# Kernel tuning notes

Hardware: AMD Instinct MI355X
Metric: run time of the kernel (lower is better)

## Reference

```python
import jax, jax.numpy as jnp
import numpy as np

# ---- fixed config (matches A_Sp_P4CNN cfg with n_channels=32) ----
C = 32          # n_channels
B = 32          # batch
H = W = 48      # input spatial size
KS = 3          # main conv kernel
SPK = 7         # spatial-attention kernel
EPS = 2e-5      # BatchNorm eps
NG = 4          # p4 rotation group size (n_grid)
SAME7 = [(SPK // 2, SPK // 2)] * 2  # 'same' padding for attention convs


def _conv2d(x, w, padding):
    return jax.lax.conv_general_dilated(
        x, w, window_strides=(1, 1), padding=padding,
        dimension_numbers=('NCHW', 'OIHW', 'NCHW'))


def _rot(w, r):
    # rotate kernel spatially by r*90 deg (p4 group action on Z2 kernels)
    return jnp.rot90(w, k=r, axes=(-2, -1))


def _gg_rot(w, r):
    # p4 action on a GG kernel [O,I,4,k,k]: spatial rotation + cyclic shift of
    # the input-rotation axis
    return jnp.roll(_rot(w, r), shift=r, axis=2)


def _lift_conv(x, w, padding):
    # lifting conv Z2 -> p4: x [B,Ci,H,W], w [Co,Ci,k,k] -> [B,Co,4,H',W']
    return jnp.stack([_conv2d(x, _rot(w, r), padding) for r in range(NG)], axis=2)


def _gg_conv(x, w, padding):
    # group conv p4 -> p4: x [B,Ci,4,H,W], w [Co,Ci,4,k,k] -> [B,Co,4,H',W']
    b, ci, g, h, ww = x.shape
    xf = x.reshape(b, ci * g, h, ww)
    outs = []
    for r in range(NG):
        wr = _gg_rot(w, r).reshape(w.shape[0], ci * g, w.shape[-2], w.shape[-1])
        outs.append(_conv2d(xf, wr, padding))
    return jnp.stack(outs, axis=2)


def _sp_att_rng(x, aw):
    # CBAM-style spatial attention lifted to p4: [B,Ci,H,W] -> [B,1,4,H,W]
    a = jnp.concatenate([jnp.mean(x, 1, keepdims=True),
                         jnp.max(x, 1, keepdims=True)], axis=1)
    return jax.nn.sigmoid(_lift_conv(a, aw, SAME7))


def _sp_att_gg(x, aw):
    # spatial attention on a p4 feature map: [B,Ci,4,H,W] -> [B,1,4,H,W]
    a = jnp.concatenate([jnp.mean(x, 1, keepdims=True),
                         jnp.max(x, 1, keepdims=True)], axis=1)
    return jax.nn.sigmoid(_gg_conv(a, aw, SAME7))


def _att_conv_rng(x, w, bias, aw):
    # attentive lifting conv: per output rotation r, modulate the input with the
    # r-th spatial attention map, then convolve with the r-rotated kernel
    att = _sp_att_rng(x, aw)  # [B,1,4,H,W]
    outs = [_conv2d(att[:, :, r] * x, _rot(w, r), 'VALID') for r in range(NG)]
    return jnp.stack(outs, axis=2) + bias[None, :, None, None, None]


def _att_conv_gg(x, w, bias, aw):
    # attentive group conv: attention broadcast over channels + input rotations
    att = _sp_att_gg(x, aw)  # [B,1,4,H,W]
    b, ci, g, h, ww = x.shape
    outs = []
    for r in range(NG):
        xr = (att[:, :, r][:, :, None] * x).reshape(b, ci * g, h, ww)
        wr = _gg_rot(w, r).reshape(w.shape[0], ci * g, KS, KS)
        outs.append(_conv2d(xr, wr, 'VALID'))
    return jnp.stack(outs, axis=2) + bias[None, :, None, None, None]


def _bn3d(x, gamma, beta):
    # BatchNorm3d over [B,C,4,H,W]: per-channel stats over (B,4,H,W) (training-mode math)
    m = jnp.mean(x, axis=(0, 2, 3, 4), keepdims=True)
    v = jnp.var(x, axis=(0, 2, 3, 4), keepdims=True)
    return gamma[None, :, None, None, None] * (x - m) * jax.lax.rsqrt(v + EPS) \
        + beta[None, :, None, None, None]


def _max_pool2(x):
    # max_pooling_Rn: 2x2/2 spatial max pool on [B,C,4,H,W]
    return jax.lax.reduce_window(x, -jnp.inf, jax.lax.max,
                                 (1, 1, 1, 2, 2), (1, 1, 1, 2, 2), 'VALID')


def setup_inputs() -> dict:
    key = jax.random.key(0)
    ks = jax.random.split(key, 40)
    sd = 0.1
    inp = {'x': jax.random.normal(ks[0], (B, 1, H, W), dtype=jnp.float32)}
    # c1: lifting conv 1 -> C
    inp['w1'] = jax.random.normal(ks[1], (C, 1, KS, KS), dtype=jnp.float32) * sd
    inp['b1'] = jnp.zeros((C,), jnp.float32)
    inp['aw1'] = jax.random.normal(ks[2], (1, 2, SPK, SPK), dtype=jnp.float32) * sd
    # c2..c6: GG convs C -> C
    for i in range(2, 7):
        inp[f'w{i}'] = jax.random.normal(ks[3 * i], (C, C, NG, KS, KS), dtype=jnp.float32) * sd
        inp[f'b{i}'] = jnp.zeros((C,), jnp.float32)
        inp[f'aw{i}'] = jax.random.normal(ks[3 * i + 1], (1, 2, NG, SPK, SPK), dtype=jnp.float32) * sd
    # c7: GG conv C -> 10 (classifier)
    inp['w7'] = jax.random.normal(ks[30], (10, C, NG, KS, KS), dtype=jnp.float32) * sd
    inp['b7'] = jnp.zeros((10,), jnp.float32)
    inp['aw7'] = jax.random.normal(ks[31], (1, 2, NG, SPK, SPK), dtype=jnp.float32) * sd
    # BatchNorm3d affine params bn1..bn6
    for i in range(1, 7):
        inp[f'g{i}'] = jnp.ones((C,), jnp.float32)
        inp[f'be{i}'] = jnp.zeros((C,), jnp.float32)
    return inp


def reference(x, w1, b1, aw1, w2, b2, aw2, w3, b3, aw3, w4, b4, aw4,
              w5, b5, aw5, w6, b6, aw6, w7, b7, aw7,
              g1, be1, g2, be2, g3, be3, g4, be4, g5, be5, g6, be6):
    # dropout is identity in eval-mode reference
    out = jax.nn.relu(_bn3d(_att_conv_rng(x, w1, b1, aw1), g1, be1))
    out = jax.nn.relu(_bn3d(_att_conv_gg(out, w2, b2, aw2), g2, be2))
    out = _max_pool2(out)
    out = jax.nn.relu(_bn3d(_att_conv_gg(out, w3, b3, aw3), g3, be3))
    out = jax.nn.relu(_bn3d(_att_conv_gg(out, w4, b4, aw4), g4, be4))
    out = jax.nn.relu(_bn3d(_att_conv_gg(out, w5, b5, aw5), g5, be5))
    out = jax.nn.relu(_bn3d(_att_conv_gg(out, w6, b6, aw6), g6, be6))
    out = _att_conv_gg(out, w7, b7, aw7)  # [B,10,4,h,w]
    out = jnp.max(out, axis=2)            # pool over rotation group (dim=-3)
    out = jnp.mean(out, axis=(2, 3))      # adaptive_avg_pool2d(1) + view
    return out                             # [B,10]
```

## Files before the change

kernel.cpp:

```cpp
#include <hip/hip_runtime.h>
#include <cstddef>

#define DINL static __device__ __forceinline__

typedef __attribute__((ext_vector_type(4))) float f4v;
typedef __attribute__((ext_vector_type(8))) short bh8;
typedef __attribute__((ext_vector_type(4))) unsigned short us4;

DINL void rot_src(int r, int K, int i, int j, int& si, int& sj) {
  switch (r & 3) {
    case 0:  si = i;       sj = j;       break;
    case 1:  si = j;       sj = K-1-i;   break;
    case 2:  si = K-1-i;   sj = K-1-j;   break;
    default: si = K-1-j;   sj = i;       break;
  }
}

DINL float sigmoidf(float s) { return 1.f / (1.f + __expf(-s)); }

DINL unsigned short f2bf(float f) {
  unsigned u = __builtin_bit_cast(unsigned, f);
  u += 0x7fffu + ((u >> 16) & 1u);
  return (unsigned short)(u >> 16);
}
DINL float bf2f(unsigned short h) {
  unsigned u = ((unsigned)h) << 16;
  return __builtin_bit_cast(float, u);
}

__global__ void k_prep_w(const float* __restrict__ w2, const float* __restrict__ w3,
                         const float* __restrict__ w4, const float* __restrict__ w5,
                         const float* __restrict__ w6, const float* __restrict__ w7,
                         unsigned short* __restrict__ wrot) {
  int idx = blockIdx.x * 256 + threadIdx.x;
  if (idx >= 811008) return;
  const float* w; int OM, O, base;
  if (idx < 737280) {
    int L = idx / 147456; base = L * 147456; OM = 2; O = 32;
    w = (L == 0) ? w2 : (L == 1) ? w3 : (L == 2) ? w4 : (L == 3) ? w5 : w6;
  } else { base = 737280; OM = 1; O = 10; w = w7; }
  int local = idx - base;
  int j = local & 7; int t = local >> 3;
  int lanei = t & 63; t >>= 6;
  int mi = t % OM; t /= OM;
  int ks = t & 3; t >>= 2;
  int tap = t % 9; int r = t / 9;
  int n = lanei & 15, q = lanei >> 4;
  int o = mi * 16 + n;
  int ci = q * 8 + j;
  int gs = (ks - r) & 3;
  int ky = tap / 3, kx = tap % 3;
  int si, sj; rot_src(r, 3, ky, kx, si, sj);
  float val = (o < O) ? w[((o * 32 + ci) * 4 + gs) * 9 + si * 3 + sj] : 0.f;
  wrot[idx] = f2bf(val);
}

DINL void bn_finalize_par(const float* __restrict__ partl,
                          const float* __restrict__ gamma, const float* __restrict__ beta,
                          float* st, float* l1, float* l2, int npix, int tid) {
  if (tid < 256) {
    int c = tid & 31, grp = tid >> 5;
    float s1 = 0.f, s2 = 0.f;
    #pragma unroll
    for (int k = 0; k < 8; ++k) {
      int bk = grp * 8 + k;
      s1 += partl[bk * 128 + c];
      s2 += partl[bk * 128 + 64 + c];
    }
    l1[tid] = s1; l2[tid] = s2;
  }
  __syncthreads();
  if (tid < 32) {
    float a = 0.f, q = 0.f;
    #pragma unroll
    for (int k = 0; k < 8; ++k) { a += l1[k * 32 + tid]; q += l2[k * 32 + tid]; }
    float N = 4.f * (float)npix;
    float m = a / N;
    float v = q / N - m * m;
    float inv = rsqrtf(v + 2e-5f);
    float sc = gamma[tid] * inv;
    st[tid] = sc;
    st[32 + tid] = beta[tid] - m * sc;
  }
  __syncthreads();
}

__global__ void __launch_bounds__(256)
k_att_lift(const float* __restrict__ x, const float* __restrict__ aw,
           float* __restrict__ att) {
  const int H = 48, HW = H * H;
  __shared__ float wsum[4][49];
  for (int i = threadIdx.x; i < 196; i += 256) {
    int r = i / 49; int t = i % 49;
    int ky = t / 7, kx = t % 7;
    int si, sj; rot_src(r, 7, ky, kx, si, sj);
    wsum[r][t] = aw[si * 7 + sj] + aw[49 + si * 7 + sj];
  }
  __syncthreads();
  int idx = blockIdx.x * 256 + threadIdx.x;
  if (idx >= 32 * 4 * HW) return;
  int xw = idx % H; int t = idx / H;
  int yh = t % H;  t /= H;
  int r  = t & 3;  int b = t >> 2;
  const float* xb = x + b * HW;
  float s = 0.f;
  for (int ky = 0; ky < 7; ++ky) {
    int y = yh + ky - 3;
    if ((unsigned)y >= (unsigned)H) continue;
    for (int kx = 0; kx < 7; ++kx) {
      int xx = xw + kx - 3;
      if ((unsigned)xx >= (unsigned)H) continue;
      s += xb[y * H + xx] * wsum[r][ky * 7 + kx];
    }
  }
  att[idx] = sigmoidf(s);
}

__global__ void __launch_bounds__(256)
k_conv_lift(const float* __restrict__ x, const float* __restrict__ att,
            const float* __restrict__ w, const float* __restrict__ bias,
            unsigned short* __restrict__ y, float* __restrict__ partl) {
  const int HO = 46;
  __shared__ float xs[3 * 48];
  __shared__ float as[4][3 * 48];
  __shared__ float wsm[288];
  __shared__ float bs[32];
  __shared__ float bnred[64];
  int id = blockIdx.x;
  int yo = id % HO; int b = id / HO;

  for (int i = threadIdx.x; i < 144; i += 256)
    xs[i] = x[b * 2304 + (yo + i / 48) * 48 + (i % 48)];
  for (int i = threadIdx.x; i < 576; i += 256) {
    int r = i / 144; int rem = i % 144;
    as[r][rem] = att[(b * 4 + r) * 2304 + (yo + rem / 48) * 48 + (rem % 48)];
  }
  for (int i = threadIdx.x; i < 288; i += 256) wsm[i] = w[i];
  if (threadIdx.x < 32) bs[threadIdx.x] = bias[threadIdx.x];
  if (threadIdx.x < 64) bnred[threadIdx.x] = 0.f;
  __syncthreads();

  int o = threadIdx.x & 31;
  int cl = threadIdx.x >> 5;
  float wreg[9];
  #pragma unroll
  for (int i = 0; i < 9; ++i) wreg[i] = wsm[o * 9 + i];
  float bv = bs[o];
  float sacc = 0.f, qacc = 0.f;

  for (int c8 = 0; c8 < 6; ++c8) {
    int col = c8 * 8 + cl;
    if (col < HO) {
      float xv[9];
      #pragma unroll
      for (int ky = 0; ky < 3; ++ky)
        #pragma unroll
        for (int kx = 0; kx < 3; ++kx)
          xv[ky * 3 + kx] = xs[ky * 48 + col + kx];
      unsigned short* yp = y + ((size_t)b * 2116 + yo * HO + col) * 128 + o;
      #pragma unroll
      for (int r = 0; r < 4; ++r) {
        float acc = bv;
        #pragma unroll
        for (int ky = 0; ky < 3; ++ky)
          #pragma unroll
          for (int kx = 0; kx < 3; ++kx) {
            int si, sj; rot_src(r, 3, ky, kx, si, sj);
            acc = fmaf(as[r][ky * 48 + col + kx] * xv[ky * 3 + kx], wreg[si * 3 + sj], acc);
          }
        yp[r * 32] = f2bf(acc);
        sacc += acc; qacc += acc * acc;
      }
    }
  }
  atomicAdd(&bnred[o], sacc);
  atomicAdd(&bnred[32 + o], qacc);
  __syncthreads();
  if (threadIdx.x < 64) {
    int bucket = blockIdx.x & 63;
    int c = threadIdx.x & 31;
    int off = (threadIdx.x < 32) ? c : (64 + c);
    atomicAdd(&partl[bucket * 128 + off], bnred[threadIdx.x]);
  }
}

template<int H, int OM, int O, int OSTR, bool BNS>
__global__ void __launch_bounds__(256)
k_conv_mfma(const unsigned short* __restrict__ xn, const float* __restrict__ att,
            const unsigned short* __restrict__ wl, const float* __restrict__ bias,
            unsigned short* __restrict__ y, float* __restrict__ partl) {
  constexpr int HO = H - 2, HW = H * H;
  constexpr int TR = 8, TC = 16, WR = TR + 2, WC = TC + 2, CGH = 68;
  constexpr int NRT = (HO + TR - 1) / TR, NCT = (HO + TC - 1) / TC;
  __shared__ __align__(16) unsigned short xa[WR * WC * CGH];
  __shared__ float bnred[128];

  int id = blockIdx.x;
  int slot = id & 7; int k = id >> 3;
  int tile = k % (NRT * NCT); k /= (NRT * NCT);
  int r = k & 3; int bhi = k >> 2;
  int b = bhi * 8 + slot;
  int rt = tile / NCT, ct = tile % NCT;
  int row0 = rt * TR, c0 = ct * TC;

  const unsigned short* xb = xn + (size_t)b * HW * 128;
  const float* ab = att + (size_t)(b * 4 + r) * HW;

  int lane = threadIdx.x & 63;
  int wv = threadIdx.x >> 6;
  int n = lane & 15, quad = lane >> 4;

  f4v acc[OM][2];
  #pragma unroll
  for (int mi = 0; mi < OM; ++mi)
    #pragma unroll
    for (int ri = 0; ri < 2; ++ri) {
      acc[mi][ri][0] = 0.f; acc[mi][ri][1] = 0.f;
      acc[mi][ri][2] = 0.f; acc[mi][ri][3] = 0.f;
    }

  const bh8* wa = (const bh8*)wl + (size_t)r * 9 * 4 * OM * 64 + lane;

  bh8 wqa[4], wqb[4];
  auto wload = [&](int s) {
    int hh = s / 18, tt = s % 18, tp = tt >> 1, kk = tt & 1, ks2 = hh * 2 + kk;
    wqa[s & 3] = wa[(size_t)((tp * 4 + ks2) * OM + 0) * 64];
    if constexpr (OM == 2)
      wqb[s & 3] = wa[(size_t)((tp * 4 + ks2) * OM + 1) * 64];
  };
  wload(0); wload(1); wload(2); wload(3);

  #pragma unroll
  for (int half = 0; half < 2; ++half) {
    if (half) __syncthreads();
    for (int u = threadIdx.x; u < WR * WC * 8; u += 256) {
      int ch = u & 7; int pix = u >> 3;
      int wr = pix / WC, wc = pix % WC;
      int row = row0 + wr; if (row > H - 1) row = H - 1;
      int col = c0 + wc;  if (col > H - 1) col = H - 1;
      int p = row * H + col;
      const unsigned short* xp = xb + (size_t)p * 128 + half * 64 + ch * 8;
      float av = ab[p];
      bh8 xv = *(const bh8*)xp;
      bh8 v;
      #pragma unroll
      for (int j2 = 0; j2 < 8; ++j2)
        v[j2] = (short)f2bf(bf2f((unsigned short)xv[j2]) * av);
      *(bh8*)&xa[pix * CGH + ch * 8] = v;
    }
    __syncthreads();

    #pragma unroll
    for (int t = 0; t < 18; ++t) {
      const int s = half * 18 + t;
      bh8 a0 = wqa[s & 3];
      bh8 a1;
      if constexpr (OM == 2) a1 = wqb[s & 3];
      if (s + 4 < 36) wload(s + 4);
      const int tap = t >> 1, kl = t & 1;
      const int ky = tap / 3, kx = tap % 3;
      int pb0 = ((2 * wv + ky) * WC + n + kx) * CGH;
      int pb1 = pb0 + WC * CGH;
      bh8 b0 = *(const bh8*)&xa[pb0 + kl * 32 + quad * 8];
      bh8 b1 = *(const bh8*)&xa[pb1 + kl * 32 + quad * 8];
      acc[0][0] = __builtin_amdgcn_mfma_f32_16x16x32_bf16(a0, b0, acc[0][0], 0, 0, 0);
      acc[0][1] = __builtin_amdgcn_mfma_f32_16x16x32_bf16(a0, b1, acc[0][1], 0, 0, 0);
      if constexpr (OM == 2) {
        acc[1][0] = __builtin_amdgcn_mfma_f32_16x16x32_bf16(a1, b0, acc[1][0], 0, 0, 0);
        acc[1][1] = __builtin_amdgcn_mfma_f32_16x16x32_bf16(a1, b1, acc[1][1], 0, 0, 0);
      }
    }
  }

  float sv[OM * 4], qv[OM * 4];
  #pragma unroll
  for (int e = 0; e < OM * 4; ++e) { sv[e] = 0.f; qv[e] = 0.f; }
  #pragma unroll
  for (int mi = 0; mi < OM; ++mi)
    #pragma unroll
    for (int ri = 0; ri < 2; ++ri) {
      int prow = row0 + 2 * wv + ri;
      int col = c0 + n;
      if (prow < HO && col < HO) {
        unsigned short* yp = y + ((size_t)b * HO * HO + prow * HO + col) * OSTR;
        int o0 = mi * 16 + quad * 4;
        f4v v = acc[mi][ri];
        if constexpr (O == 32) {
          us4 w4;
          #pragma unroll
          for (int reg = 0; reg < 4; ++reg) {
            float val = v[reg] + bias[o0 + reg];
            w4[reg] = f2bf(val);
            if constexpr (BNS) { sv[mi * 4 + reg] += val; qv[mi * 4 + reg] += val * val; }
          }
          *(us4*)(yp + r * 32 + o0) = w4;
        } else {
          #pragma unroll
          for (int reg = 0; reg < 4; ++reg) {
            int o = o0 + reg;
            if (o < O) yp[r * O + o] = f2bf(v[reg] + bias[o]);
          }
        }
      }
    }

  if constexpr (BNS) {
    #pragma unroll
    for (int e = 0; e < OM * 4; ++e) {
      #pragma unroll
      for (int off = 1; off < 16; off <<= 1) {
        sv[e] += __shfl_xor(sv[e], off);
        qv[e] += __shfl_xor(qv[e], off);
      }
    }
    if (threadIdx.x < 128) bnred[threadIdx.x] = 0.f;
    __syncthreads();
    if (n == 0) {
      #pragma unroll
      for (int e = 0; e < OM * 4; ++e) {
        int o = (e >> 2) * 16 + quad * 4 + (e & 3);
        atomicAdd(&bnred[o], sv[e]);
        atomicAdd(&bnred[64 + o], qv[e]);
      }
    }
    __syncthreads();
    if (threadIdx.x < 128)
      atomicAdd(&partl[(blockIdx.x & 63) * 128 + threadIdx.x], bnred[threadIdx.x]);
  }
}

__global__ void __launch_bounds__(256)
k_meanmax_bn(const unsigned short* __restrict__ yr, const float* __restrict__ partl,
             const float* __restrict__ gamma, const float* __restrict__ beta,
             unsigned short* __restrict__ xn, unsigned short* __restrict__ amap,
             int npix) {
  __shared__ float st[64];
  __shared__ float l1[256], l2[256];
  bn_finalize_par(partl, gamma, beta, st, l1, l2, npix, threadIdx.x);
  int idx = blockIdx.x * 256 + threadIdx.x;
  if (idx >= npix) return;
  const unsigned short* yp = yr + (size_t)idx * 128;
  unsigned short* xp = xn + (size_t)idx * 128;
  float sm[4] = {0.f, 0.f, 0.f, 0.f};
  float mx[4] = {-1e30f, -1e30f, -1e30f, -1e30f};
  #pragma unroll 4
  for (int oo = 0; oo < 16; ++oo) {
    int g = oo >> 2, ob = (oo & 3) * 8;
    bh8 raw = *(const bh8*)(yp + oo * 8);
    bh8 w;
    #pragma unroll
    for (int e = 0; e < 8; ++e) {
      float v = fmaxf(fmaf(bf2f((unsigned short)raw[e]), st[ob + e], st[32 + ob + e]), 0.f);
      w[e] = (short)f2bf(v);
      sm[g] += v;
      mx[g] = fmaxf(mx[g], v);
    }
    *(bh8*)(xp + oo * 8) = w;
  }
  bh8 am;
  #pragma unroll
  for (int g = 0; g < 4; ++g) {
    am[g] = (short)f2bf(sm[g] * (1.f / 32.f));
    am[4 + g] = (short)f2bf(mx[g]);
  }
  *(bh8*)(amap + (size_t)idx * 8) = am;
}

template<int HIN, int HOUT, bool POOL>
__global__ void __launch_bounds__(256)
k_postA(const unsigned short* __restrict__ yr, const float* __restrict__ partl,
        const float* __restrict__ gamma, const float* __restrict__ beta,
        unsigned short* __restrict__ xn, unsigned short* __restrict__ amap) {
  __shared__ float st[64];
  __shared__ float l1[256], l2[256];
  bn_finalize_par(partl, gamma, beta, st, l1, l2, 32 * HIN * HIN, threadIdx.x);
  int idx = blockIdx.x * 256 + threadIdx.x;
  if (idx >= 32 * HOUT * HOUT * 4) return;
  int g = idx & 3; int p = idx >> 2;
  int col = p % HOUT; int t = p / HOUT;
  int row = t % HOUT; int b = t / HOUT;
  float sm = 0.f, mx = -1e30f;
  unsigned short* xp = xn + (size_t)p * 128 + g * 32;
  if constexpr (POOL) {
    const unsigned short* p00 =
        yr + ((size_t)b * HIN * HIN + (row * 2) * HIN + col * 2) * 128 + g * 32;
    #pragma unroll
    for (int k = 0; k < 4; ++k) {
      bh8 r0 = *(const bh8*)(p00 + k * 8);
      bh8 r1 = *(const bh8*)(p00 + 128 + k * 8);
      bh8 r2 = *(const bh8*)(p00 + (size_t)HIN * 128 + k * 8);
      bh8 r3 = *(const bh8*)(p00 + (size_t)(HIN + 1) * 128 + k * 8);
      bh8 w;
      #pragma unroll
      for (int e = 0; e < 8; ++e) {
        float sc = st[k * 8 + e], sh = st[32 + k * 8 + e];
        float a0 = fmaxf(fmaf(bf2f((unsigned short)r0[e]), sc, sh), 0.f);
        float a1 = fmaxf(fmaf(bf2f((unsigned short)r1[e]), sc, sh), 0.f);
        float a2 = fmaxf(fmaf(bf2f((unsigned short)r2[e]), sc, sh), 0.f);
        float a3 = fmaxf(fmaf(bf2f((unsigned short)r3[e]), sc, sh), 0.f);
        float val = fmaxf(fmaxf(a0, a1), fmaxf(a2, a3));
        w[e] = (short)f2bf(val);
        sm += val; mx = fmaxf(mx, val);
      }
      *(bh8*)(xp + k * 8) = w;
    }
  } else {
    const unsigned short* yp = yr + (size_t)p * 128 + g * 32;
    #pragma unroll
    for (int k = 0; k < 4; ++k) {
      bh8 raw = *(const bh8*)(yp + k * 8);
      bh8 w;
      #pragma unroll
      for (int e = 0; e < 8; ++e) {
        float v = fmaxf(fmaf(bf2f((unsigned short)raw[e]), st[k * 8 + e], st[32 + k * 8 + e]), 0.f);
        w[e] = (short)f2bf(v);
        sm += v;
        mx = fmaxf(mx, v);
      }
      *(bh8*)(xp + k * 8) = w;
    }
  }
  amap[(size_t)p * 8 + g] = f2bf(sm * (1.f / 32.f));
  amap[(size_t)p * 8 + 4 + g] = f2bf(mx);
}

__global__ void __launch_bounds__(256)
k_att_gg(const unsigned short* __restrict__ amap, const float* __restrict__ aw,
         float* __restrict__ att, int h) {
  __shared__ float wsa[4][4][49], wsx[4][4][49];
  for (int i = threadIdx.x; i < 784; i += 256) {
    int r = i / 196; int rem = i % 196;
    int g = rem / 49; int t = rem % 49;
    int ky = t / 7, kx = t % 7;
    int si, sj; rot_src(r, 7, ky, kx, si, sj);
    int gs = (g - r) & 3;
    wsa[r][g][t] = aw[gs * 49 + si * 7 + sj];
    wsx[r][g][t] = aw[(4 + gs) * 49 + si * 7 + sj];
  }
  __syncthreads();
  int hw = h * h;
  int idx = blockIdx.x * 256 + threadIdx.x;
  if (idx >= 32 * 4 * hw) return;
  int p = idx % hw; int t = idx / hw;
  int r = t & 3; int b = t >> 2;
  int yh = p / h, xw = p % h;
  float s = 0.f;
  for (int ky = 0; ky < 7; ++ky) {
    int y = yh + ky - 3;
    if ((unsigned)y >= (unsigned)h) continue;
    for (int kx = 0; kx < 7; ++kx) {
      int xx = xw + kx - 3;
      if ((unsigned)xx >= (unsigned)h) continue;
      int tp = ky * 7 + kx;
      bh8 av = *(const bh8*)(amap + ((size_t)b * hw + y * h + xx) * 8);
      #pragma unroll
      for (int g = 0; g < 4; ++g)
        s += bf2f((unsigned short)av[g]) * wsa[r][g][tp]
           + bf2f((unsigned short)av[4 + g]) * wsx[r][g][tp];
    }
  }
  att[idx] = sigmoidf(s);
}

__global__ void k_final(const unsigned short* __restrict__ y7, float* __restrict__ out) {
  int idx = blockIdx.x * blockDim.x + threadIdx.x;
  if (idx >= 320) return;
  int o = idx % 10; int b = idx / 10;
  const unsigned short* p = y7 + (size_t)b * 144 * 40;
  float s = 0.f;
  for (int sp = 0; sp < 144; ++sp) {
    const unsigned short* q = p + sp * 40 + o;
    float m = fmaxf(fmaxf(bf2f(q[0]), bf2f(q[10])), fmaxf(bf2f(q[20]), bf2f(q[30])));
    s += m;
  }
  out[idx] = s * (1.f / 144.f);
}


extern "C" void kernel_launch(void* const* d_in, const int* in_sizes, int n_in,
                              void* d_out, int out_size, void* d_ws, size_t ws_size,
                              hipStream_t stream) {
  (void)in_sizes; (void)n_in; (void)out_size; (void)ws_size;
  const float* x   = (const float*)d_in[0];
  const float* w1  = (const float*)d_in[1];
  const float* b1  = (const float*)d_in[2];
  const float* aw1 = (const float*)d_in[3];
  const float* W[6];  const float* BI[6]; const float* AW[6];
  for (int i = 0; i < 6; ++i) {
    W[i]  = (const float*)d_in[4 + 3 * i];
    BI[i] = (const float*)d_in[5 + 3 * i];
    AW[i] = (const float*)d_in[6 + 3 * i];
  }
  const float* G[6]; const float* BE[6];
  for (int i = 0; i < 6; ++i) {
    G[i]  = (const float*)d_in[22 + 2 * i];
    BE[i] = (const float*)d_in[23 + 2 * i];
  }
  float* out = (float*)d_out;

  float* ws = (float*)d_ws;
  unsigned short* YR = (unsigned short*)ws;
  unsigned short* XN = (unsigned short*)(ws + 4333568);
  unsigned short* AMAP = (unsigned short*)(ws + 8667136);
  float* ATT = ws + 8937984;
  unsigned short* WROT = (unsigned short*)(ws + 9232896);
  float* PART  = ws + 9638400;

  auto cdiv = [](int a, int b) { return (a + b - 1) / b; };
  float* PL[6];
  for (int i = 0; i < 6; ++i) PL[i] = PART + i * 8192;

  hipMemsetAsync(PART, 0, 6 * 8192 * sizeof(float), stream);

  k_prep_w<<<dim3(cdiv(811008, 256)), dim3(256), 0, stream>>>(
      W[0], W[1], W[2], W[3], W[4], W[5], WROT);
  const unsigned short* WL[6];
  for (int i = 0; i < 5; ++i) WL[i] = WROT + i * 147456;
  WL[5] = WROT + 737280;

  {
    int natt = 32 * 4 * 48 * 48;
    k_att_lift<<<dim3(cdiv(natt, 256)), dim3(256), 0, stream>>>(x, aw1, ATT);
    k_conv_lift<<<dim3(32 * 46), dim3(256), 0, stream>>>(x, ATT, w1, b1, YR, PL[0]);
    int npix = 32 * 2116;
    k_meanmax_bn<<<dim3(cdiv(npix, 256)), dim3(256), 0, stream>>>(YR, PL[0], G[0], BE[0], XN, AMAP, npix);
    k_att_gg<<<dim3(cdiv(npix * 4, 256)), dim3(256), 0, stream>>>(AMAP, AW[0], ATT, 46);
  }
  k_conv_mfma<46, 2, 32, 128, true><<<dim3(128 * 6 * 3), dim3(256), 0, stream>>>(XN, ATT, WL[0], BI[0], YR, PL[1]);
  k_postA<44, 22, true><<<dim3(cdiv(32 * 22 * 22 * 4, 256)), dim3(256), 0, stream>>>(YR, PL[1], G[1], BE[1], XN, AMAP);
  k_att_gg<<<dim3(cdiv(32 * 4 * 22 * 22, 256)), dim3(256), 0, stream>>>(AMAP, AW[1], ATT, 22);
  k_conv_mfma<22, 2, 32, 128, true><<<dim3(128 * 3 * 2), dim3(256), 0, stream>>>(XN, ATT, WL[1], BI[1], YR, PL[2]);
  k_postA<20, 20, false><<<dim3(cdiv(32 * 20 * 20 * 4, 256)), dim3(256), 0, stream>>>(YR, PL[2], G[2], BE[2], XN, AMAP);
  k_att_gg<<<dim3(cdiv(32 * 4 * 20 * 20, 256)), dim3(256), 0, stream>>>(AMAP, AW[2], ATT, 20);
  k_conv_mfma<20, 2, 32, 128, true><<<dim3(128 * 3 * 2), dim3(256), 0, stream>>>(XN, ATT, WL[2], BI[2], YR, PL[3]);
  k_postA<18, 18, false><<<dim3(cdiv(32 * 18 * 18 * 4, 256)), dim3(256), 0, stream>>>(YR, PL[3], G[3], BE[3], XN, AMAP);
  k_att_gg<<<dim3(cdiv(32 * 4 * 18 * 18, 256)), dim3(256), 0, stream>>>(AMAP, AW[3], ATT, 18);
  k_conv_mfma<18, 2, 32, 128, true><<<dim3(128 * 2 * 1), dim3(256), 0, stream>>>(XN, ATT, WL[3], BI[3], YR, PL[4]);
  k_postA<16, 16, false><<<dim3(cdiv(32 * 16 * 16 * 4, 256)), dim3(256), 0, stream>>>(YR, PL[4], G[4], BE[4], XN, AMAP);
  k_att_gg<<<dim3(cdiv(32 * 4 * 16 * 16, 256)), dim3(256), 0, stream>>>(AMAP, AW[4], ATT, 16);
  k_conv_mfma<16, 2, 32, 128, true><<<dim3(128 * 2 * 1), dim3(256), 0, stream>>>(XN, ATT, WL[4], BI[4], YR, PL[5]);
  k_postA<14, 14, false><<<dim3(cdiv(32 * 14 * 14 * 4, 256)), dim3(256), 0, stream>>>(YR, PL[5], G[5], BE[5], XN, AMAP);
  k_att_gg<<<dim3(cdiv(32 * 4 * 14 * 14, 256)), dim3(256), 0, stream>>>(AMAP, AW[5], ATT, 14);
  k_conv_mfma<14, 1, 10, 40, false><<<dim3(128 * 2 * 1), dim3(256), 0, stream>>>(XN, ATT, WL[5], BI[5], YR, nullptr);
  k_final<<<dim3(5), dim3(64), 0, stream>>>(YR, out);
}
```

Baseline: 427.8 us.

## Double-buffer LDS input tile to overlap second-half loads with first-half MFMAs

Splits the attention-modulated input staging into an issue phase (global loads into registers) and a write phase (scale, convert, store to LDS). A two-buffer shared array lets the second channel half's global loads be in flight while the first half's MFMA loop runs, and drops one barrier. It doubles the LDS footprint and adds live registers for the prefetched data, which may reduce occupancy.

Measured after the change: 408.0 us. 1.05x faster.

```diff
diff --git a/kernel.cpp b/kernel.cpp
--- a/kernel.cpp
+++ b/kernel.cpp
@@ -192,7 +192,10 @@
   constexpr int HO = H - 2, HW = H * H;
   constexpr int TR = 8, TC = 16, WR = TR + 2, WC = TC + 2, CGH = 68;
   constexpr int NRT = (HO + TR - 1) / TR, NCT = (HO + TC - 1) / TC;
-  __shared__ __align__(16) unsigned short xa[WR * WC * CGH];
+  constexpr int NPIX = WR * WC;
+  constexpr int NCH = NPIX * 8;
+  constexpr int NST = (NCH + 255) / 256;
+  __shared__ __align__(16) unsigned short xa[2][NPIX * CGH];
   __shared__ float bnred[128];
 
   int id = blockIdx.x;
@@ -206,8 +209,9 @@
   const unsigned short* xb = xn + (size_t)b * HW * 128;
   const float* ab = att + (size_t)(b * 4 + r) * HW;
 
-  int lane = threadIdx.x & 63;
-  int wv = threadIdx.x >> 6;
+  int tid = threadIdx.x;
+  int lane = tid & 63;
+  int wv = tid >> 6;
   int n = lane & 15, quad = lane >> 4;
 
   f4v acc[OM][2];
@@ -228,28 +232,38 @@
     if constexpr (OM == 2)
       wqb[s & 3] = wa[(size_t)((tp * 4 + ks2) * OM + 1) * 64];
   };
-  wload(0); wload(1); wload(2); wload(3);
-
-  #pragma unroll
-  for (int half = 0; half < 2; ++half) {
-    if (half) __syncthreads();
-    for (int u = threadIdx.x; u < WR * WC * 8; u += 256) {
-      int ch = u & 7; int pix = u >> 3;
-      int wr = pix / WC, wc = pix % WC;
-      int row = row0 + wr; if (row > H - 1) row = H - 1;
-      int col = c0 + wc;  if (col > H - 1) col = H - 1;
-      int p = row * H + col;
-      const unsigned short* xp = xb + (size_t)p * 128 + half * 64 + ch * 8;
-      float av = ab[p];
-      bh8 xv = *(const bh8*)xp;
-      bh8 v;
-      #pragma unroll
-      for (int j2 = 0; j2 < 8; ++j2)
-        v[j2] = (short)f2bf(bf2f((unsigned short)xv[j2]) * av);
-      *(bh8*)&xa[pix * CGH + ch * 8] = v;
-    }
-    __syncthreads();
-
+
+  bh8 sx[NST]; float sa[NST];
+  auto issue = [&](int half) {
+    #pragma unroll
+    for (int i = 0; i < NST; ++i) {
+      int u = tid + i * 256;
+      if (i + 1 < NST || u < NCH) {
+        int ch = u & 7; int pix = u >> 3;
+        int wr = pix / WC, wc = pix % WC;
+        int row = row0 + wr; if (row > H - 1) row = H - 1;
+        int col = c0 + wc;  if (col > H - 1) col = H - 1;
+        int p = row * H + col;
+        sx[i] = *(const bh8*)(xb + (size_t)p * 128 + half * 64 + ch * 8);
+        sa[i] = ab[p];
+      }
+    }
+  };
+  auto wlds = [&](int half) {
+    #pragma unroll
+    for (int i = 0; i < NST; ++i) {
+      int u = tid + i * 256;
+      if (i + 1 < NST || u < NCH) {
+        int ch = u & 7; int pix = u >> 3;
+        bh8 v;
+        #pragma unroll
+        for (int j2 = 0; j2 < 8; ++j2)
+          v[j2] = (short)f2bf(bf2f((unsigned short)sx[i][j2]) * sa[i]);
+        *(bh8*)&xa[half][pix * CGH + ch * 8] = v;
+      }
+    }
+  };
+  auto mfma_half = [&](int half) {
     #pragma unroll
     for (int t = 0; t < 18; ++t) {
       const int s = half * 18 + t;
@@ -261,8 +275,8 @@
       const int ky = tap / 3, kx = tap % 3;
       int pb0 = ((2 * wv + ky) * WC + n + kx) * CGH;
       int pb1 = pb0 + WC * CGH;
-      bh8 b0 = *(const bh8*)&xa[pb0 + kl * 32 + quad * 8];
-      bh8 b1 = *(const bh8*)&xa[pb1 + kl * 32 + quad * 8];
+      bh8 b0 = *(const bh8*)&xa[half][pb0 + kl * 32 + quad * 8];
+      bh8 b1 = *(const bh8*)&xa[half][pb1 + kl * 32 + quad * 8];
       acc[0][0] = __builtin_amdgcn_mfma_f32_16x16x32_bf16(a0, b0, acc[0][0], 0, 0, 0);
       acc[0][1] = __builtin_amdgcn_mfma_f32_16x16x32_bf16(a0, b1, acc[0][1], 0, 0, 0);
       if constexpr (OM == 2) {
@@ -270,7 +284,17 @@
         acc[1][1] = __builtin_amdgcn_mfma_f32_16x16x32_bf16(a1, b1, acc[1][1], 0, 0, 0);
       }
     }
-  }
+  };
+
+  wload(0); wload(1); wload(2); wload(3);
+  issue(0);
+  wlds(0);
+  __syncthreads();
+  issue(1);
+  mfma_half(0);
+  wlds(1);
+  __syncthreads();
+  mfma_half(1);
 
   float sv[OM * 4], qv[OM * 4];
   #pragma unroll
```
